# Kernel optimization log

Measured on AMD Instinct MI355X. Metric: run time of the kernel, lower is better.

## Reference

```python
import jax, jax.numpy as jnp
import numpy as np

IN_FEATURES = 4096
OUT_FEATURES = 4096
K = 0.5  # keep top-k fraction of weights by |score|


def setup_inputs() -> dict:
    key = jax.random.key(0)
    kx, kw, ks = jax.random.split(key, 3)
    x = jax.random.normal(kx, (8192, IN_FEATURES), dtype=jnp.float32)
    # kaiming_normal_(mode='fan_in', nonlinearity='relu'): std = sqrt(2/fan_in)
    std = float(np.sqrt(2.0 / IN_FEATURES))
    weights = jax.random.normal(kw, (OUT_FEATURES, IN_FEATURES), dtype=jnp.float32) * std
    bias = jnp.zeros((OUT_FEATURES,), dtype=jnp.float32)
    # scores init to ones in torch, but perturb so the top-k selection is non-degenerate
    scores = jnp.ones((OUT_FEATURES, IN_FEATURES), dtype=jnp.float32) + 0.01 * jax.random.normal(ks, (OUT_FEATURES, IN_FEATURES), dtype=jnp.float32)
    return {"x": x, "weights": weights, "bias": bias, "scores": scores}


def _topk_mask(s):
    # Reproduces torch sort-based thresholding: flatten, sort ascending,
    # bottom j = int((1-K)*n) entries -> 0, remaining top entries -> 1.
    flat = s.ravel()
    n = flat.shape[0]
    j = int((1.0 - K) * n)
    order = jnp.argsort(flat)  # ascending
    keep = (jnp.arange(n) >= j).astype(s.dtype)
    mask_flat = jnp.zeros((n,), dtype=s.dtype).at[order].set(keep)
    return mask_flat.reshape(s.shape)


def reference(x, weights, bias, scores):
    s = jnp.abs(scores)
    hard = _topk_mask(s)
    # straight-through estimator: forward uses hard mask, grad passes to |scores|
    mask = s + jax.lax.stop_gradient(hard - s)
    pruned = weights * mask  # [out, in]
    return x @ pruned.T + bias  # [B, out]
```

## Files before the change

kernel.cpp:

```cpp
#include <hip/hip_runtime.h>


#define NTOT   16777216u
#define JDROP  8388608u
#define MDIM   8192
#define NDIM   4096
#define KDIM   4096

typedef __bf16 v8bf __attribute__((ext_vector_type(8)));
typedef float  v4f  __attribute__((ext_vector_type(4)));

__device__ __forceinline__ unsigned short f2bf(float f){
  unsigned u = __float_as_uint(f);
  u += 0x7fffu + ((u >> 16) & 1u);
  return (unsigned short)(u >> 16);
}

__global__ void zero_hist(unsigned* hist){ hist[threadIdx.x] = 0u; }

__global__ __launch_bounds__(256) void hist_pass(const float* __restrict__ scores,
                                                 unsigned* __restrict__ hist,
                                                 const unsigned* __restrict__ state,
                                                 int p){
  __shared__ __align__(16) unsigned char pc[256*256];
  int tid = threadIdx.x;
  unsigned* pz = (unsigned*)pc;
  #pragma unroll
  for (int k=0;k<64;++k) pz[tid + k*256] = 0u;
  __syncthreads();
  unsigned prefix = (p>0) ? state[0] : 0u;
  const float4* s4 = (const float4*)(scores + (size_t)blockIdx.x * 16384);
  for (int it=0; it<16; ++it){
    float4 v = s4[(size_t)it*256 + tid];
    #pragma unroll
    for (int e=0;e<4;++e){
      float f = (e==0)?v.x:(e==1)?v.y:(e==2)?v.z:v.w;
      unsigned u = __float_as_uint(f) & 0x7fffffffu;
      unsigned d, ok;
      if      (p==0){ d = u>>23;         ok = 1u; }
      else if (p==1){ d = (u>>15)&0xffu; ok = ((u>>23)==prefix); }
      else if (p==2){ d = (u>>7) &0xffu; ok = ((u>>15)==prefix); }
      else          { d = u & 0x7fu;     ok = ((u>>7) ==prefix); }
      if (ok) pc[d*256 + tid]++;
    }
  }
  __syncthreads();
  unsigned b = (unsigned)tid;
  const unsigned* row = (const unsigned*)(pc + b*256);
  unsigned s = 0;
  for (int kk=0;kk<64;++kk){
    int k = (kk + tid) & 63;
    unsigned w = row[k];
    s += (w & 0xffu) + ((w>>8)&0xffu) + ((w>>16)&0xffu) + (w>>24);
  }
  if (s) atomicAdd(&hist[b], s);
}

__global__ void select_pass(unsigned* hist, unsigned* state, int p){
  int lane = threadIdx.x;
  unsigned c[4];
  #pragma unroll
  for (int k=0;k<4;++k){ c[k] = hist[lane*4+k]; hist[lane*4+k] = 0u; }
  unsigned s = c[0]+c[1]+c[2]+c[3];
  unsigned inc = s;
  #pragma unroll
  for (int d=1; d<64; d<<=1){
    unsigned t = (unsigned)__shfl_up((int)inc, d, 64);
    if (lane >= d) inc += t;
  }
  unsigned excl = inc - s;
  unsigned target = (p==0) ? JDROP : state[1];
  unsigned oldpre = (p==0) ? 0u    : state[0];
  if (target >= excl && target < excl + s){
    unsigned cum = excl, digit = 0, below = 0;
    #pragma unroll
    for (int k=0;k<4;++k){
      if (target < cum + c[k]){ digit = (unsigned)lane*4u + (unsigned)k; below = cum; break; }
      cum += c[k];
    }
    state[0] = (oldpre << ((p==3)?7:8)) | digit;
    state[1] = target - below;
  }
}

__global__ __launch_bounds__(256) void tie_count(const float* __restrict__ scores,
                                                 const unsigned* __restrict__ state,
                                                 unsigned* __restrict__ tieCnt){
  unsigned T = state[0];
  int tid = threadIdx.x;
  const float4* s4 = (const float4*)(scores + (size_t)blockIdx.x * 4096);
  unsigned cnt = 0;
  for (int it=0; it<4; ++it){
    float4 v = s4[it*256 + tid];
    #pragma unroll
    for (int e=0;e<4;++e){
      float f = (e==0)?v.x:(e==1)?v.y:(e==2)?v.z:v.w;
      unsigned u = __float_as_uint(f) & 0x7fffffffu;
      cnt += (u == T) ? 1u : 0u;
    }
  }
  __shared__ unsigned r[256];
  r[tid] = cnt; __syncthreads();
  for (int s=128; s>0; s>>=1){ if (tid < s) r[tid] += r[tid+s]; __syncthreads(); }
  if (tid==0) tieCnt[blockIdx.x] = r[0];
}

__global__ __launch_bounds__(1024) void tie_scan(const unsigned* tieCnt, unsigned* tieBase){
  int tid = threadIdx.x;
  unsigned v[4], pre[4], s = 0;
  #pragma unroll
  for (int k=0;k<4;++k){ v[k] = tieCnt[tid*4+k]; pre[k] = s; s += v[k]; }
  __shared__ unsigned sc[1024];
  sc[tid] = s; __syncthreads();
  for (int d=1; d<1024; d<<=1){
    unsigned t = (tid >= d) ? sc[tid-d] : 0u;
    __syncthreads();
    sc[tid] += t;
    __syncthreads();
  }
  unsigned excl = sc[tid] - s;
  #pragma unroll
  for (int k=0;k<4;++k) tieBase[tid*4+k] = excl + pre[k];
}

__global__ __launch_bounds__(256) void build_pruned(const float* __restrict__ scores,
                                                    const float* __restrict__ w,
                                                    const unsigned* __restrict__ state,
                                                    const unsigned* __restrict__ tieBase,
                                                    unsigned short* __restrict__ wpr){
  int c = blockIdx.x;
  int tid = threadIdx.x;
  int lane = tid & 63, wid = tid >> 6;
  unsigned T = state[0], D = state[1];
  __shared__ unsigned wcnt[4];
  __shared__ unsigned runBase;
  if (tid==0) runBase = tieBase[c];
  size_t base = (size_t)c * 4096;
  for (int it=0; it<16; ++it){
    size_t i = base + it*256 + tid;
    unsigned u = __float_as_uint(scores[i]) & 0x7fffffffu;
    bool tie = (u == T), gt = (u > T);
    unsigned long long b = __ballot(tie);
    unsigned lanePre = (unsigned)__popcll(b & ((1ull << lane) - 1ull));
    if (lane==0) wcnt[wid] = (unsigned)__popcll(b);
    __syncthreads();
    unsigned off = 0;
    #pragma unroll
    for (int ww=0; ww<4; ++ww) if (ww < wid) off += wcnt[ww];
    unsigned tot = wcnt[0]+wcnt[1]+wcnt[2]+wcnt[3];
    unsigned rank = runBase + off + lanePre;
    bool keep = gt || (tie && rank >= D);
    wpr[i] = keep ? f2bf(w[i]) : (unsigned short)0;
    __syncthreads();
    if (tid==0) runBase += tot;
  }
}

__global__ __launch_bounds__(256) void convert_x(const float4* __restrict__ x,
                                                 ushort4* __restrict__ xb){
  size_t i = (size_t)blockIdx.x * 256 + threadIdx.x;
  float4 v = x[i];
  ushort4 o; o.x=f2bf(v.x); o.y=f2bf(v.y); o.z=f2bf(v.z); o.w=f2bf(v.w);
  xb[i] = o;
}

__device__ __forceinline__ void gload_lds16b(const void* g, void* l){
  __builtin_amdgcn_global_load_lds(
      (__attribute__((address_space(1))) void*)g,
      (__attribute__((address_space(3))) void*)l, 16, 0, 0);
}

__device__ __forceinline__ void stage_mat(const unsigned short* __restrict__ G, int rowBase,
                                          unsigned short (* __restrict__ S)[64],
                                          int kt, int wid, int lane){
  #pragma unroll
  for (int hj=0; hj<4; ++hj){
    const int rg0 = (hj>>1)*128 + (wid*2 + (hj&1))*8;
    const int rg  = rg0 + (lane>>3);
    const int c16 = (lane&7) ^ (rg & 7);
    gload_lds16b(G + (size_t)(rowBase + rg)*KDIM + kt*64 + c16*8, &S[rg0][0]);
  }
}

__device__ __forceinline__ v8bf ldsfrag(const unsigned short (* __restrict__ S)[64],
                                        int row, int kc){
  return *(const v8bf*)&S[row][(kc ^ (row & 7))*8];
}

#define BAR()   { __builtin_amdgcn_s_barrier(); asm volatile("" ::: "memory"); }
#define LGKM0() asm volatile("s_waitcnt lgkmcnt(0)" ::: "memory")

__device__ __forceinline__ void ktile(const unsigned short* __restrict__ A,
                                      const unsigned short* __restrict__ B,
                                      unsigned short (* __restrict__ Asq)[64],
                                      unsigned short (* __restrict__ Bsq)[64],
                                      int Mb, int Nb, int t,
                                      int wr, int wc, int wid, int lane,
                                      v4f acc[8][4]){
  const int r16 = lane & 15, kg = lane >> 4;
  const bool pf = (t + 2 < KDIM/64);

  v8bf a0[4][2], b0[2][2];
  #pragma unroll
  for (int i=0;i<4;++i)
    #pragma unroll
    for (int ks=0;ks<2;++ks)
      a0[i][ks] = ldsfrag(Asq, wr*128 + i*16 + r16, ks*4 + kg);
  #pragma unroll
  for (int n=0;n<2;++n)
    #pragma unroll
    for (int ks=0;ks<2;++ks)
      b0[n][ks] = ldsfrag(Bsq, wc*64 + n*16 + r16, ks*4 + kg);
  BAR(); LGKM0();
  __builtin_amdgcn_s_setprio(1);
  #pragma unroll
  for (int i=0;i<4;++i)
    #pragma unroll
    for (int n=0;n<2;++n)
      #pragma unroll
      for (int ks=0;ks<2;++ks)
        acc[i][n] = __builtin_amdgcn_mfma_f32_16x16x32_bf16(a0[i][ks], b0[n][ks], acc[i][n], 0,0,0);
  __builtin_amdgcn_s_setprio(0);
  BAR();

  v8bf b1[2][2];
  #pragma unroll
  for (int n=0;n<2;++n)
    #pragma unroll
    for (int ks=0;ks<2;++ks)
      b1[n][ks] = ldsfrag(Bsq, wc*64 + (2+n)*16 + r16, ks*4 + kg);
  BAR(); LGKM0();
  __builtin_amdgcn_s_setprio(1);
  #pragma unroll
  for (int i=0;i<4;++i)
    #pragma unroll
    for (int n=0;n<2;++n)
      #pragma unroll
      for (int ks=0;ks<2;++ks)
        acc[i][2+n] = __builtin_amdgcn_mfma_f32_16x16x32_bf16(a0[i][ks], b1[n][ks], acc[i][2+n], 0,0,0);
  __builtin_amdgcn_s_setprio(0);
  BAR();

  v8bf a1[4][2];
  #pragma unroll
  for (int i=0;i<4;++i)
    #pragma unroll
    for (int ks=0;ks<2;++ks)
      a1[i][ks] = ldsfrag(Asq, wr*128 + 64 + i*16 + r16, ks*4 + kg);
  if (pf) stage_mat(B, Nb, Bsq, t+2, wid, lane);
  BAR(); LGKM0();
  __builtin_amdgcn_s_setprio(1);
  #pragma unroll
  for (int i=0;i<4;++i)
    #pragma unroll
    for (int n=0;n<2;++n)
      #pragma unroll
      for (int ks=0;ks<2;++ks)
        acc[4+i][n] = __builtin_amdgcn_mfma_f32_16x16x32_bf16(a1[i][ks], b0[n][ks], acc[4+i][n], 0,0,0);
  __builtin_amdgcn_s_setprio(0);
  BAR();

  if (pf) stage_mat(A, Mb, Asq, t+2, wid, lane);
  __builtin_amdgcn_s_setprio(1);
  #pragma unroll
  for (int i=0;i<4;++i)
    #pragma unroll
    for (int n=0;n<2;++n)
      #pragma unroll
      for (int ks=0;ks<2;++ks)
        acc[4+i][2+n] = __builtin_amdgcn_mfma_f32_16x16x32_bf16(a1[i][ks], b1[n][ks], acc[4+i][2+n], 0,0,0);
  __builtin_amdgcn_s_setprio(0);
  if (pf) { asm volatile("s_waitcnt vmcnt(8)" ::: "memory"); }
  else    { asm volatile("s_waitcnt vmcnt(0)" ::: "memory"); }
  BAR();
}

__global__ __launch_bounds__(512, 2) void gemm256(const unsigned short* __restrict__ A,
                                                  const unsigned short* __restrict__ B,
                                                  const float* __restrict__ bias,
                                                  float* __restrict__ out){
  __shared__ __align__(16) unsigned short As[2][256][64];
  __shared__ __align__(16) unsigned short Bs[2][256][64];

  const int bid = blockIdx.x;
  const int swz = (bid & 7) * 64 + (bid >> 3);
  const int Mb  = (swz >> 4) * 256;
  const int Nb  = (swz & 15) * 256;

  const int tid  = threadIdx.x;
  const int lane = tid & 63;
  const int wid  = tid >> 6;
  const int wr   = wid >> 2;
  const int wc   = wid & 3;

  v4f acc[8][4];
  #pragma unroll
  for (int i=0;i<8;++i)
    #pragma unroll
    for (int n=0;n<4;++n) acc[i][n] = (v4f){0.f,0.f,0.f,0.f};

  stage_mat(A, Mb, As[0], 0, wid, lane);
  stage_mat(B, Nb, Bs[0], 0, wid, lane);
  stage_mat(A, Mb, As[1], 1, wid, lane);
  stage_mat(B, Nb, Bs[1], 1, wid, lane);
  asm volatile("s_waitcnt vmcnt(8)" ::: "memory");
  BAR();

  #pragma unroll 1
  for (int t = 0; t < KDIM/64; t += 2){
    ktile(A, B, As[0], Bs[0], Mb, Nb, t,   wr, wc, wid, lane, acc);
    ktile(A, B, As[1], Bs[1], Mb, Nb, t+1, wr, wc, wid, lane, acc);
  }

  #pragma unroll
  for (int mt=0; mt<8; ++mt){
    const int gm0 = Mb + wr*128 + mt*16 + (lane >> 4)*4;
    #pragma unroll
    for (int nt=0; nt<4; ++nt){
      const int gn = Nb + wc*64 + nt*16 + (lane & 15);
      const float bv = bias[gn];
      v4f a = acc[mt][nt];
      #pragma unroll
      for (int r=0; r<4; ++r)
        out[(size_t)(gm0 + r)*NDIM + gn] = a[r] + bv;
    }
  }
}

extern "C" void kernel_launch(void* const* d_in, const int* in_sizes, int n_in,
                              void* d_out, int out_size, void* d_ws, size_t ws_size,
                              hipStream_t stream){
  const float* x      = (const float*)d_in[0];
  const float* w      = (const float*)d_in[1];
  const float* bias   = (const float*)d_in[2];
  const float* scores = (const float*)d_in[3];
  float* out = (float*)d_out;

  char* ws = (char*)d_ws;
  unsigned* hist    = (unsigned*)(ws);
  unsigned* state   = (unsigned*)(ws + 1024);
  unsigned* tieCnt  = (unsigned*)(ws + 2048);
  unsigned* tieBase = (unsigned*)(ws + 2048 + 16384);
  unsigned short* xb  = (unsigned short*)(ws + 65536);
  unsigned short* wpr = (unsigned short*)(ws + 65536 + (size_t)MDIM*KDIM*2);

  zero_hist<<<1, 256, 0, stream>>>(hist);
  for (int p = 0; p < 4; ++p){
    hist_pass<<<1024, 256, 0, stream>>>(scores, hist, state, p);
    select_pass<<<1, 64, 0, stream>>>(hist, state, p);
  }
  tie_count<<<4096, 256, 0, stream>>>(scores, state, tieCnt);
  tie_scan<<<1, 1024, 0, stream>>>(tieCnt, tieBase);
  build_pruned<<<4096, 256, 0, stream>>>(scores, w, state, tieBase, wpr);
  convert_x<<<MDIM*KDIM/4/256, 256, 0, stream>>>((const float4*)x, (ushort4*)xb);

  gemm256<<<dim3(512), 512, 0, stream>>>(xb, wpr, bias, out);
}
```

Before: 754.4 us.

## Prefetch next k-tile MFMA fragments in GEMM and vectorize per-row mask build

The GEMM k-tile routine now loads the next tile's A/B register fragments from the alternate LDS buffer at the end of the current tile. This removes several barriers and lgkmcnt waits between LDS reads and MFMA blocks, so LDS latency overlaps with compute. Separately, build_pruned now assigns one wavefront per row and uses float4 loads and ushort4 stores. Tie ranks are computed with per-wave ballots instead of block-wide shared memory and __syncthreads. The cost is higher register pressure from carrying fragments across tiles, and more dependence on compiler-inserted waits for LDS ordering.

```diff
diff --git a/kernel.cpp b/kernel.cpp
--- a/kernel.cpp
+++ b/kernel.cpp
@@ -128,31 +128,41 @@
                                                     const unsigned* __restrict__ state,
                                                     const unsigned* __restrict__ tieBase,
                                                     unsigned short* __restrict__ wpr){
-  int c = blockIdx.x;
-  int tid = threadIdx.x;
-  int lane = tid & 63, wid = tid >> 6;
-  unsigned T = state[0], D = state[1];
-  __shared__ unsigned wcnt[4];
-  __shared__ unsigned runBase;
-  if (tid==0) runBase = tieBase[c];
-  size_t base = (size_t)c * 4096;
+  const int row  = blockIdx.x*4 + (threadIdx.x >> 6);
+  const int lane = threadIdx.x & 63;
+  const unsigned T = state[0], D = state[1];
+  unsigned runBase = tieBase[row];
+  const float4* s4 = (const float4*)(scores + (size_t)row*4096);
+  const float4* w4 = (const float4*)(w      + (size_t)row*4096);
+  ushort4*      o4 = (ushort4*)(wpr + (size_t)row*4096);
+  const unsigned long long below = (lane==0)?0ull:((~0ull) >> (64-lane));
   for (int it=0; it<16; ++it){
-    size_t i = base + it*256 + tid;
-    unsigned u = __float_as_uint(scores[i]) & 0x7fffffffu;
-    bool tie = (u == T), gt = (u > T);
-    unsigned long long b = __ballot(tie);
-    unsigned lanePre = (unsigned)__popcll(b & ((1ull << lane) - 1ull));
-    if (lane==0) wcnt[wid] = (unsigned)__popcll(b);
-    __syncthreads();
-    unsigned off = 0;
-    #pragma unroll
-    for (int ww=0; ww<4; ++ww) if (ww < wid) off += wcnt[ww];
-    unsigned tot = wcnt[0]+wcnt[1]+wcnt[2]+wcnt[3];
-    unsigned rank = runBase + off + lanePre;
-    bool keep = gt || (tie && rank >= D);
-    wpr[i] = keep ? f2bf(w[i]) : (unsigned short)0;
-    __syncthreads();
-    if (tid==0) runBase += tot;
+    float4 sv = s4[it*64 + lane];
+    float4 wv = w4[it*64 + lane];
+    unsigned u0 = __float_as_uint(sv.x) & 0x7fffffffu;
+    unsigned u1 = __float_as_uint(sv.y) & 0x7fffffffu;
+    unsigned u2 = __float_as_uint(sv.z) & 0x7fffffffu;
+    unsigned u3 = __float_as_uint(sv.w) & 0x7fffffffu;
+    bool t0=(u0==T), t1=(u1==T), t2=(u2==T), t3=(u3==T);
+    unsigned long long b0=__ballot(t0), b1=__ballot(t1), b2=__ballot(t2), b3=__ballot(t3);
+    unsigned lanesBelow = (unsigned)(__popcll(b0&below)+__popcll(b1&below)
+                                   + __popcll(b2&below)+__popcll(b3&below));
+    unsigned base = runBase + lanesBelow;
+    unsigned r0 = base;
+    unsigned r1 = base + (t0?1u:0u);
+    unsigned r2 = r1   + (t1?1u:0u);
+    unsigned r3 = r2   + (t2?1u:0u);
+    bool k0 = (u0>T) || (t0 && r0>=D);
+    bool k1 = (u1>T) || (t1 && r1>=D);
+    bool k2 = (u2>T) || (t2 && r2>=D);
+    bool k3 = (u3>T) || (t3 && r3>=D);
+    ushort4 o;
+    o.x = k0 ? f2bf(wv.x) : (unsigned short)0;
+    o.y = k1 ? f2bf(wv.y) : (unsigned short)0;
+    o.z = k2 ? f2bf(wv.z) : (unsigned short)0;
+    o.w = k3 ? f2bf(wv.w) : (unsigned short)0;
+    o4[it*64 + lane] = o;
+    runBase += (unsigned)(__popcll(b0)+__popcll(b1)+__popcll(b2)+__popcll(b3));
   }
 }
 
@@ -188,30 +198,26 @@
 }
 
 #define BAR()   { __builtin_amdgcn_s_barrier(); asm volatile("" ::: "memory"); }
-#define LGKM0() asm volatile("s_waitcnt lgkmcnt(0)" ::: "memory")
 
 __device__ __forceinline__ void ktile(const unsigned short* __restrict__ A,
                                       const unsigned short* __restrict__ B,
                                       unsigned short (* __restrict__ Asq)[64],
                                       unsigned short (* __restrict__ Bsq)[64],
+                                      unsigned short (* __restrict__ AsqN)[64],
+                                      unsigned short (* __restrict__ BsqN)[64],
                                       int Mb, int Nb, int t,
                                       int wr, int wc, int wid, int lane,
-                                      v4f acc[8][4]){
+                                      v4f acc[8][4], v8bf a0[4][2], v8bf b0[2][2]){
   const int r16 = lane & 15, kg = lane >> 4;
   const bool pf = (t + 2 < KDIM/64);
-
-  v8bf a0[4][2], b0[2][2];
-  #pragma unroll
-  for (int i=0;i<4;++i)
+  const bool nx = (t + 1 < KDIM/64);
+
+  v8bf b1[2][2];
+  #pragma unroll
+  for (int n=0;n<2;++n)
     #pragma unroll
     for (int ks=0;ks<2;++ks)
-      a0[i][ks] = ldsfrag(Asq, wr*128 + i*16 + r16, ks*4 + kg);
-  #pragma unroll
-  for (int n=0;n<2;++n)
-    #pragma unroll
-    for (int ks=0;ks<2;++ks)
-      b0[n][ks] = ldsfrag(Bsq, wc*64 + n*16 + r16, ks*4 + kg);
-  BAR(); LGKM0();
+      b1[n][ks] = ldsfrag(Bsq, wc*64 + (2+n)*16 + r16, ks*4 + kg);
   __builtin_amdgcn_s_setprio(1);
   #pragma unroll
   for (int i=0;i<4;++i)
@@ -221,15 +227,13 @@
       for (int ks=0;ks<2;++ks)
         acc[i][n] = __builtin_amdgcn_mfma_f32_16x16x32_bf16(a0[i][ks], b0[n][ks], acc[i][n], 0,0,0);
   __builtin_amdgcn_s_setprio(0);
-  BAR();
-
-  v8bf b1[2][2];
-  #pragma unroll
-  for (int n=0;n<2;++n)
+
+  v8bf a1[4][2];
+  #pragma unroll
+  for (int i=0;i<4;++i)
     #pragma unroll
     for (int ks=0;ks<2;++ks)
-      b1[n][ks] = ldsfrag(Bsq, wc*64 + (2+n)*16 + r16, ks*4 + kg);
-  BAR(); LGKM0();
+      a1[i][ks] = ldsfrag(Asq, wr*128 + 64 + i*16 + r16, ks*4 + kg);
   __builtin_amdgcn_s_setprio(1);
   #pragma unroll
   for (int i=0;i<4;++i)
@@ -241,14 +245,7 @@
   __builtin_amdgcn_s_setprio(0);
   BAR();
 
-  v8bf a1[4][2];
-  #pragma unroll
-  for (int i=0;i<4;++i)
-    #pragma unroll
-    for (int ks=0;ks<2;++ks)
-      a1[i][ks] = ldsfrag(Asq, wr*128 + 64 + i*16 + r16, ks*4 + kg);
   if (pf) stage_mat(B, Nb, Bsq, t+2, wid, lane);
-  BAR(); LGKM0();
   __builtin_amdgcn_s_setprio(1);
   #pragma unroll
   for (int i=0;i<4;++i)
@@ -273,6 +270,19 @@
   if (pf) { asm volatile("s_waitcnt vmcnt(8)" ::: "memory"); }
   else    { asm volatile("s_waitcnt vmcnt(0)" ::: "memory"); }
   BAR();
+
+  if (nx){
+    #pragma unroll
+    for (int i=0;i<4;++i)
+      #pragma unroll
+      for (int ks=0;ks<2;++ks)
+        a0[i][ks] = ldsfrag(AsqN, wr*128 + i*16 + r16, ks*4 + kg);
+    #pragma unroll
+    for (int n=0;n<2;++n)
+      #pragma unroll
+      for (int ks=0;ks<2;++ks)
+        b0[n][ks] = ldsfrag(BsqN, wc*64 + n*16 + r16, ks*4 + kg);
+  }
 }
 
 __global__ __launch_bounds__(512, 2) void gemm256(const unsigned short* __restrict__ A,
@@ -292,6 +302,7 @@
   const int wid  = tid >> 6;
   const int wr   = wid >> 2;
   const int wc   = wid & 3;
+  const int r16  = lane & 15, kg = lane >> 4;
 
   v4f acc[8][4];
   #pragma unroll
@@ -306,10 +317,22 @@
   asm volatile("s_waitcnt vmcnt(8)" ::: "memory");
   BAR();
 
+  v8bf a0[4][2], b0[2][2];
+  #pragma unroll
+  for (int i=0;i<4;++i)
+    #pragma unroll
+    for (int ks=0;ks<2;++ks)
+      a0[i][ks] = ldsfrag(As[0], wr*128 + i*16 + r16, ks*4 + kg);
+  #pragma unroll
+  for (int n=0;n<2;++n)
+    #pragma unroll
+    for (int ks=0;ks<2;++ks)
+      b0[n][ks] = ldsfrag(Bs[0], wc*64 + n*16 + r16, ks*4 + kg);
+
   #pragma unroll 1
   for (int t = 0; t < KDIM/64; t += 2){
-    ktile(A, B, As[0], Bs[0], Mb, Nb, t,   wr, wc, wid, lane, acc);
-    ktile(A, B, As[1], Bs[1], Mb, Nb, t+1, wr, wc, wid, lane, acc);
+    ktile(A, B, As[0], Bs[0], As[1], Bs[1], Mb, Nb, t,   wr, wc, wid, lane, acc, a0, b0);
+    ktile(A, B, As[1], Bs[1], As[0], Bs[0], Mb, Nb, t+1, wr, wc, wid, lane, acc, a0, b0);
   }
 
   #pragma unroll
@@ -351,7 +374,7 @@
   }
   tie_count<<<4096, 256, 0, stream>>>(scores, state, tieCnt);
   tie_scan<<<1, 1024, 0, stream>>>(tieCnt, tieBase);
-  build_pruned<<<4096, 256, 0, stream>>>(scores, w, state, tieBase, wpr);
+  build_pruned<<<1024, 256, 0, stream>>>(scores, w, state, tieBase, wpr);
   convert_x<<<MDIM*KDIM/4/256, 256, 0, stream>>>((const float4*)x, (ushort4*)xb);
 
   gemm256<<<dim3(512), 512, 0, stream>>>(xb, wpr, bias, out);
```

Result: slower. 888.9 us (+17.8%).
